# Kernel optimization log

Measured on AMD Instinct MI355X. Metric: run time of the kernel, lower is better.

## Reference

```python
import jax, jax.numpy as jnp
import numpy as np

D_MODEL = 128
N_HEADS = 8
RES_SCALE = 2.0 ** (-0.5)  # self_normalizing residual scale

OCC = np.array([65,66,67,68,69,70,71,72,73,74,75,76,77,81,82,83,84,88,89,90,94], dtype=np.int64)


def conv1d_same(x, w, groups=1):
    # x: [B, Cin, T], w: [Cout, Cin//groups, K] -> [B, Cout, T], 'same' padding, no bias
    return jax.lax.conv_general_dilated(
        x, w, window_strides=(1,), padding='SAME',
        dimension_numbers=('NCH', 'OIH', 'NCH'),
        feature_group_count=groups)


def setup_inputs() -> dict:
    key = jax.random.key(0)
    ks = jax.random.split(key, 7)
    B, C, T = 8, 128, 500
    L, D, O, K = 2, D_MODEL, 21, 9
    def lecun(k, shape, fan_in):
        return jax.random.normal(k, shape, dtype=jnp.float32) / jnp.sqrt(jnp.float32(fan_in))
    return {
        'x': jax.random.normal(ks[0], (B, C, T), dtype=jnp.float32),
        'occ_idx': jnp.asarray(OCC),
        'wq': lecun(ks[1], (L, D, O, K), O * K),
        'wk': lecun(ks[2], (L, C * D, 1, K), K),
        'wv': lecun(ks[3], (L, C * D, 1, K), K),
        'wproj': lecun(ks[4], (L, C, D), D),
        'w_head': lecun(ks[5], (40, C * T), C * T),
        'b_head': jnp.zeros((40,), dtype=jnp.float32),
    }


def reference(x, occ_idx, wq, wk, wv, wproj, w_head, b_head):
    B, C, T = x.shape
    L = wq.shape[0]
    H, D = N_HEADS, D_MODEL
    d = D // H  # head dim
    scale = d ** (-0.5)
    selu = jax.nn.selu
    for l in range(L):
        x_occ = x[:, occ_idx]                               # [B, O, T]
        Q = selu(conv1d_same(x_occ, wq[l]))                 # [B, D, T]
        K = selu(conv1d_same(x, wk[l], groups=C))           # [B, C*D, T]
        V = selu(conv1d_same(x, wv[l], groups=C))           # [B, C*D, T]
        Qh = Q.reshape(B, H, d, T)                          # b (h d) t -> b h d t
        Kh = K.reshape(B, C, H, d, T).transpose(0, 2, 1, 3, 4)  # b h c d t
        Vh = V.reshape(B, C, H, d, T).transpose(0, 2, 1, 3, 4)
        gates = selu(jnp.einsum('bhdt,bhcdt->bhct', Qh, Kh) * scale)
        out = jnp.einsum('bhct,bhcdt->bhcdt', gates, Vh)    # [B, H, C, d, T]
        out = out.transpose(0, 2, 1, 3, 4).reshape(B, C, D, T)  # b (c h d) t grouped by c
        # grouped 1x1 conv (groups=C): per-channel projection D -> 1
        out = selu(jnp.einsum('bcdt,cd->bct', out, wproj[l]))
        x = (x + out) * RES_SCALE
    logits = x.reshape(B, -1) @ w_head.T + b_head           # [B, n_classes]
    return logits
```

## Files before the change

kernel.cpp:

```cpp
#include <hip/hip_runtime.h>
#include <math.h>

#define T_LEN   500
#define C_CH    128
#define DM      128
#define N_OCC   21
#define KSZ     9
#define N_OUT   40
#define LOG2E   1.44269504088896340736f

typedef _Float16 f16x8 __attribute__((ext_vector_type(8)));
typedef _Float16 f16x2 __attribute__((ext_vector_type(2)));
typedef float    f32x16 __attribute__((ext_vector_type(16)));

union pair_u { unsigned int u; f16x2 h; };

__device__ __forceinline__ float exp2_fast(float y) {
#if __has_builtin(__builtin_amdgcn_exp2f)
    return __builtin_amdgcn_exp2f(y);
#else
    return exp2f(y);
#endif
}

__device__ __forceinline__ float selu2(float y) {
    const float c1 = 0.7282904300f;
    const float la = 1.7580993408473766f;
    float e = exp2_fast(y);
    return y > 0.f ? c1 * y : fmaf(la, e, -la);
}

__device__ __forceinline__ f32x16 zero16() {
    f32x16 z;
#pragma unroll
    for (int j = 0; j < 16; ++j) z[j] = 0.f;
    return z;
}

__global__ void prep_kernel(const float* __restrict__ wq,
                            const float* __restrict__ wk, const float* __restrict__ wv,
                            float* __restrict__ wqT,
                            _Float16* __restrict__ wkh, _Float16* __restrict__ wvh)
{
    int idx = blockIdx.x * 256 + threadIdx.x;
    if (idx < 2 * N_OCC * KSZ * DM) {
        int D  = idx & 127;
        int r  = idx >> 7;
        int k  = r % KSZ;
        int r2 = r / KSZ;
        int o  = r2 % N_OCC;
        int l  = r2 / N_OCC;
        wqT[idx] = wq[(((size_t)l * DM + D) * N_OCC + o) * KSZ + k] * LOG2E;
    }
    if (idx < 2 * C_CH * 4 * 64) {
        int lane = idx & 63;
        int ch   = (idx >> 6) & 3;
        int c    = (idx >> 8) & 127;
        int l    = idx >> 15;
        int tcol = lane & 31, hi = lane >> 5;
        int D    = ch * 32 + tcol;
        const float* wkp = wk + ((size_t)l * C_CH * DM + (size_t)c * DM + D) * KSZ;
        const float* wvp = wv + ((size_t)l * C_CH * DM + (size_t)c * DM + D) * KSZ;
#pragma unroll
        for (int j = 0; j < 8; ++j) {
            int k = 8 * hi + j;
            wkh[(size_t)idx * 8 + j] = (k < KSZ) ? (_Float16)(wkp[k] * LOG2E) : (_Float16)0.f;
            wvh[(size_t)idx * 8 + j] = (k < KSZ) ? (_Float16)(wvp[k] * LOG2E) : (_Float16)0.f;
        }
    }
}

#define ATCH 8
__global__ __launch_bounds__(128) void qconv_kernel(
    const float* __restrict__ xin, const int* __restrict__ occ,
    const float* __restrict__ wqT, float* __restrict__ qtP, int l)
{
    const int b  = blockIdx.y;
    const int t0 = blockIdx.x * ATCH;
    const int D  = threadIdx.x;
    __shared__ float xo[N_OCC][ATCH + 8];
    for (int i = threadIdx.x; i < N_OCC * (ATCH + 8); i += 128) {
        int o = i / (ATCH + 8), j = i % (ATCH + 8);
        int tg = t0 + j - 4;
        xo[o][j] = (tg >= 0 && tg < T_LEN)
                     ? xin[((size_t)b * C_CH + occ[o]) * T_LEN + tg] : 0.f;
    }
    __syncthreads();

    float acc[ATCH];
#pragma unroll
    for (int tt = 0; tt < ATCH; ++tt) acc[tt] = 0.f;

    for (int o = 0; o < N_OCC; ++o) {
        float xr[ATCH + 8];
#pragma unroll
        for (int j = 0; j < ATCH + 8; ++j) xr[j] = xo[o][j];
#pragma unroll
        for (int k = 0; k < KSZ; ++k) {
            float w = wqT[(((size_t)l * N_OCC + o) * KSZ + k) * DM + D];
#pragma unroll
            for (int tt = 0; tt < ATCH; ++tt)
                acc[tt] = fmaf(xr[tt + k], w, acc[tt]);
        }
    }
    const int tile = t0 >> 5, tl = t0 & 31;
    const int ch = D >> 5, w = D & 31;
    const int g  = 2 * (w >> 3) + ((w >> 2) & 1);
    const int i2 = w & 3;
    float* qb = qtP + ((((size_t)(b * 16 + tile) * 4 + ch) * 8 + g) * 32 + tl) * 4 + i2;
#pragma unroll
    for (int tt = 0; tt < ATCH; ++tt)
        if (t0 + tt < T_LEN) qb[tt * 4] = selu2(acc[tt]);
}

__global__ __launch_bounds__(256) void fused_layer(
    const float* __restrict__ xin, const float* __restrict__ qtP,
    const f16x8* __restrict__ wkh, const f16x8* __restrict__ wvh,
    const float* __restrict__ wproj, float* __restrict__ xout, int l)
{
    const int c = blockIdx.x, b = blockIdx.y;
    const int tid  = threadIdx.x;
    const int wave = tid >> 6;
    const int lane = tid & 63;
    const int tcol = lane & 31;
    const int hi   = lane >> 5;

    const f16x8* wkf = wkh + ((size_t)(l * C_CH + c) * 4) * 64 + lane;
    const f16x8* wvf = wvh + ((size_t)(l * C_CH + c) * 4) * 64 + lane;
    f16x8 ak[4], av[4];
#pragma unroll
    for (int ch = 0; ch < 4; ++ch) {
        ak[ch] = wkf[ch * 64];
        av[ch] = wvf[ch * 64];
    }

    __shared__ float xs[528];
    __shared__ unsigned int xs2[527];
    __shared__ float wpj[DM];
    const float* xp = xin + ((size_t)(b * C_CH + c)) * T_LEN;
    for (int i = tid; i < 528; i += 256) {
        int tg = i - 4;
        float a0 = (tg >= 0 && tg < T_LEN) ? xp[tg] : 0.f;
        float a1 = (tg + 1 >= 0 && tg + 1 < T_LEN) ? xp[tg + 1] : 0.f;
        xs[i] = a0;
        if (i < 527) {
            pair_u p;
            p.h[0] = (_Float16)a0;
            p.h[1] = (_Float16)a1;
            xs2[i] = p.u;
        }
    }
    if (tid < DM) wpj[tid] = wproj[((size_t)l * C_CH + c) * DM + tid];
    __syncthreads();

#define LOADQ(p0, p1, p2, p3, chv, tilev) do {                                \
    const float4* qp_ = reinterpret_cast<const float4*>(qtP)                  \
        + (((size_t)(b * 16 + (tilev)) * 4 + (chv)) * 8) * 32 + tcol;         \
    p0 = qp_[(0 + hi) * 32];                                                  \
    p1 = qp_[(2 + hi) * 32];                                                  \
    p2 = qp_[(4 + hi) * 32];                                                  \
    p3 = qp_[(6 + hi) * 32];                                                  \
} while (0)

#define KPROC(chv, p0, p1, p2, p3) do {                                       \
    f32x16 acc_ = zero16();                                                   \
    acc_ = __builtin_amdgcn_mfma_f32_32x32x16_f16(ak[chv], bfr, acc_, 0, 0, 0);\
    float pA = 0.f, pB = 0.f;                                                 \
    pA = fmaf(p0.x, selu2(acc_[0]),  pA);                                     \
    pA = fmaf(p0.y, selu2(acc_[1]),  pA);                                     \
    pA = fmaf(p0.z, selu2(acc_[2]),  pA);                                     \
    pA = fmaf(p0.w, selu2(acc_[3]),  pA);                                     \
    pA = fmaf(p1.x, selu2(acc_[4]),  pA);                                     \
    pA = fmaf(p1.y, selu2(acc_[5]),  pA);                                     \
    pA = fmaf(p1.z, selu2(acc_[6]),  pA);                                     \
    pA = fmaf(p1.w, selu2(acc_[7]),  pA);                                     \
    pB = fmaf(p2.x, selu2(acc_[8]),  pB);                                     \
    pB = fmaf(p2.y, selu2(acc_[9]),  pB);                                     \
    pB = fmaf(p2.z, selu2(acc_[10]), pB);                                     \
    pB = fmaf(p2.w, selu2(acc_[11]), pB);                                     \
    pB = fmaf(p3.x, selu2(acc_[12]), pB);                                     \
    pB = fmaf(p3.y, selu2(acc_[13]), pB);                                     \
    pB = fmaf(p3.z, selu2(acc_[14]), pB);                                     \
    pB = fmaf(p3.w, selu2(acc_[15]), pB);                                     \
    qk[(chv) * 2 + 0] += pA;                                                  \
    qk[(chv) * 2 + 1] += pB;                                                  \
} while (0)

    float4 qa0, qa1, qa2, qa3, qb0, qb1, qb2, qb3;
    LOADQ(qa0, qa1, qa2, qa3, 0, wave * 4);
    LOADQ(qb0, qb1, qb2, qb3, 1, wave * 4);

#pragma unroll 1
    for (int ti = 0; ti < 4; ++ti) {
        const int tile = wave * 4 + ti;
        const int loc0 = tile * 32;
        const int t    = loc0 + tcol;

        f16x8 bfr;
        {
            const int base = loc0 + tcol + 8 * hi;
#pragma unroll
            for (int j = 0; j < 4; ++j) {
                pair_u p; p.u = xs2[base + 2 * j];
                bfr[2 * j]     = p.h[0];
                bfr[2 * j + 1] = p.h[1];
            }
        }

        float qk[8];
#pragma unroll
        for (int h = 0; h < 8; ++h) qk[h] = 0.f;

        KPROC(0, qa0, qa1, qa2, qa3);
        LOADQ(qa0, qa1, qa2, qa3, 2, tile);
        KPROC(1, qb0, qb1, qb2, qb3);
        LOADQ(qb0, qb1, qb2, qb3, 3, tile);
        KPROC(2, qa0, qa1, qa2, qa3);
        KPROC(3, qb0, qb1, qb2, qb3);

        float g[8];
#pragma unroll
        for (int h = 0; h < 8; ++h) {
            float full = qk[h] + __shfl_xor(qk[h], 32);
            g[h] = selu2(full * (0.25f * LOG2E));
        }

        const int ntile = (ti < 3) ? tile + 1 : tile;
        LOADQ(qa0, qa1, qa2, qa3, 0, ntile);
        LOADQ(qb0, qb1, qb2, qb3, 1, ntile);

        float outp = 0.f;
#pragma unroll
        for (int ch = 0; ch < 4; ++ch) {
            f32x16 acc = zero16();
            acc = __builtin_amdgcn_mfma_f32_32x32x16_f16(av[ch], bfr, acc, 0, 0, 0);
            float sA = 0.f, sB = 0.f;
#pragma unroll
            for (int I = 0; I < 4; ++I) {
                float4 wq4 = *reinterpret_cast<const float4*>(
                    &wpj[(ch * 8 + 2 * I + hi) * 4]);
#pragma unroll
                for (int i2 = 0; i2 < 4; ++i2) {
                    float vv = selu2(acc[4 * I + i2]);
                    if (I < 2) sA = fmaf((&wq4.x)[i2], vv, sA);
                    else       sB = fmaf((&wq4.x)[i2], vv, sB);
                }
            }
            outp = fmaf(g[ch * 2 + 0], sA, outp);
            outp = fmaf(g[ch * 2 + 1], sB, outp);
        }
        float outf = outp + __shfl_xor(outp, 32);

        if (hi == 0 && t < T_LEN) {
            const float rs = 0.70710678118654752f;
            xout[((size_t)(b * C_CH + c)) * T_LEN + t]
                = (xs[loc0 + tcol + 4] + selu2(outf * LOG2E)) * rs;
        }
    }
#undef LOADQ
#undef KPROC
}

#define NCHUNK 16
#define CHUNK  (C_CH * T_LEN / NCHUNK)
__global__ __launch_bounds__(256) void head_partial(
    const float* __restrict__ x, const float* __restrict__ wh,
    float* __restrict__ part)
{
    const int o  = blockIdx.x;
    const int ch = blockIdx.y;
    const int base = ch * CHUNK;
    const float4* wp = reinterpret_cast<const float4*>(wh + (size_t)o * (C_CH * T_LEN) + base);

    float acc[8];
#pragma unroll
    for (int b = 0; b < 8; ++b) acc[b] = 0.f;

    for (int i = threadIdx.x; i < CHUNK / 4; i += 256) {
        float4 w4 = wp[i];
#pragma unroll
        for (int b = 0; b < 8; ++b) {
            float4 x4 = reinterpret_cast<const float4*>(
                x + (size_t)b * (C_CH * T_LEN) + base)[i];
            acc[b] = fmaf(x4.x, w4.x, acc[b]);
            acc[b] = fmaf(x4.y, w4.y, acc[b]);
            acc[b] = fmaf(x4.z, w4.z, acc[b]);
            acc[b] = fmaf(x4.w, w4.w, acc[b]);
        }
    }

#pragma unroll
    for (int b = 0; b < 8; ++b)
#pragma unroll
        for (int off = 32; off > 0; off >>= 1)
            acc[b] += __shfl_down(acc[b], off);

    __shared__ float red[4][8];
    const int lane = threadIdx.x & 63, wid = threadIdx.x >> 6;
    if (lane == 0)
#pragma unroll
        for (int b = 0; b < 8; ++b) red[wid][b] = acc[b];
    __syncthreads();
    if (threadIdx.x < 8) {
        int b = threadIdx.x;
        part[((size_t)o * NCHUNK + ch) * 8 + b]
            = red[0][b] + red[1][b] + red[2][b] + red[3][b];
    }
}

__global__ __launch_bounds__(320) void head_final(
    const float* __restrict__ part, const float* __restrict__ bh,
    float* __restrict__ out)
{
    int i = threadIdx.x;
    if (i >= N_OUT * 8) return;
    int o = i >> 3, b = i & 7;
    float s = bh[o];
#pragma unroll
    for (int ch = 0; ch < NCHUNK; ++ch)
        s += part[((size_t)o * NCHUNK + ch) * 8 + b];
    out[b * N_OUT + o] = s;
}

extern "C" void kernel_launch(void* const* d_in, const int* in_sizes, int n_in,
                              void* d_out, int out_size, void* d_ws, size_t ws_size,
                              hipStream_t stream) {
    const float* x     = (const float*)d_in[0];
    const int*   occ   = (const int*)  d_in[1];
    const float* wq    = (const float*)d_in[2];
    const float* wk    = (const float*)d_in[3];
    const float* wv    = (const float*)d_in[4];
    const float* wproj = (const float*)d_in[5];
    const float* wh    = (const float*)d_in[6];
    const float* bh    = (const float*)d_in[7];
    float* out = (float*)d_out;

    float* ws  = (float*)d_ws;
    float* wqT = ws;
    float* qtb = wqT + 2 * N_OCC * KSZ * DM;
    float* xb0 = qtb + (size_t)8 * 16 * DM * 32;
    float* xb1 = xb0 + (size_t)8 * C_CH * T_LEN;
    float* hp  = xb1 + (size_t)8 * C_CH * T_LEN;
    _Float16* wkh = (_Float16*)(hp + N_OUT * NCHUNK * 8);
    _Float16* wvh = wkh + (size_t)2 * C_CH * 4 * 64 * 8;

    prep_kernel<<<dim3(256), 256, 0, stream>>>(wq, wk, wv, wqT, wkh, wvh);

    qconv_kernel<<<dim3(63, 8), 128, 0, stream>>>(x, occ, wqT, qtb, 0);
    fused_layer <<<dim3(128, 8), 256, 0, stream>>>(
        x, qtb, (const f16x8*)wkh, (const f16x8*)wvh, wproj, xb0, 0);

    qconv_kernel<<<dim3(63, 8), 128, 0, stream>>>(xb0, occ, wqT, qtb, 1);
    fused_layer <<<dim3(128, 8), 256, 0, stream>>>(
        xb0, qtb, (const f16x8*)wkh, (const f16x8*)wvh, wproj, xb1, 1);

    head_partial<<<dim3(N_OUT, NCHUNK), 256, 0, stream>>>(xb1, wh, hp);
    head_final  <<<dim3(1), 320, 0, stream>>>(hp, bh, out);
}
```

Measured before the change: 112.5 us.

## Split fused layer over time halves and fold head reduction into atomics

The fused attention layer now launches twice as many blocks, each handling half of the time axis with two tiles per wave instead of four. This is meant to raise occupancy across the GPU's compute units, at the cost of duplicating the per-block weight register loads and halo staging. The Q prefetch schedule is reordered to suit the shorter loop. The two-kernel head is also replaced by a memset plus one kernel that accumulates partials with atomicAdd, which removes a launch but makes the float summation order nondeterministic.

```diff
diff --git a/kernel.cpp b/kernel.cpp
--- a/kernel.cpp
+++ b/kernel.cpp
@@ -118,7 +118,7 @@
     const f16x8* __restrict__ wkh, const f16x8* __restrict__ wvh,
     const float* __restrict__ wproj, float* __restrict__ xout, int l)
 {
-    const int c = blockIdx.x, b = blockIdx.y;
+    const int c = blockIdx.x, b = blockIdx.y, zi = blockIdx.z;
     const int tid  = threadIdx.x;
     const int wave = tid >> 6;
     const int lane = tid & 63;
@@ -134,16 +134,16 @@
         av[ch] = wvf[ch * 64];
     }
 
-    __shared__ float xs[528];
-    __shared__ unsigned int xs2[527];
+    __shared__ float xs[272];
+    __shared__ unsigned int xs2[271];
     __shared__ float wpj[DM];
     const float* xp = xin + ((size_t)(b * C_CH + c)) * T_LEN;
-    for (int i = tid; i < 528; i += 256) {
-        int tg = i - 4;
+    for (int i = tid; i < 272; i += 256) {
+        int tg = zi * 256 + i - 4;
         float a0 = (tg >= 0 && tg < T_LEN) ? xp[tg] : 0.f;
         float a1 = (tg + 1 >= 0 && tg + 1 < T_LEN) ? xp[tg + 1] : 0.f;
         xs[i] = a0;
-        if (i < 527) {
+        if (i < 271) {
             pair_u p;
             p.h[0] = (_Float16)a0;
             p.h[1] = (_Float16)a1;
@@ -187,14 +187,15 @@
 } while (0)
 
     float4 qa0, qa1, qa2, qa3, qb0, qb1, qb2, qb3;
-    LOADQ(qa0, qa1, qa2, qa3, 0, wave * 4);
-    LOADQ(qb0, qb1, qb2, qb3, 1, wave * 4);
+    LOADQ(qa0, qa1, qa2, qa3, 0, zi * 8 + wave * 2);
 
 #pragma unroll 1
-    for (int ti = 0; ti < 4; ++ti) {
-        const int tile = wave * 4 + ti;
-        const int loc0 = tile * 32;
-        const int t    = loc0 + tcol;
+    for (int ti = 0; ti < 2; ++ti) {
+        const int tile = zi * 8 + wave * 2 + ti;
+        const int loc0 = wave * 64 + ti * 32;
+        const int t    = zi * 256 + loc0 + tcol;
+
+        LOADQ(qb0, qb1, qb2, qb3, 1, tile);
 
         f16x8 bfr;
         {
@@ -216,6 +217,8 @@
         KPROC(1, qb0, qb1, qb2, qb3);
         LOADQ(qb0, qb1, qb2, qb3, 3, tile);
         KPROC(2, qa0, qa1, qa2, qa3);
+        const int ntile = (ti < 1) ? tile + 1 : tile;
+        LOADQ(qa0, qa1, qa2, qa3, 0, ntile);
         KPROC(3, qb0, qb1, qb2, qb3);
 
         float g[8];
@@ -224,10 +227,6 @@
             float full = qk[h] + __shfl_xor(qk[h], 32);
             g[h] = selu2(full * (0.25f * LOG2E));
         }
-
-        const int ntile = (ti < 3) ? tile + 1 : tile;
-        LOADQ(qa0, qa1, qa2, qa3, 0, ntile);
-        LOADQ(qb0, qb1, qb2, qb3, 1, ntile);
 
         float outp = 0.f;
 #pragma unroll
@@ -263,9 +262,9 @@
 
 #define NCHUNK 16
 #define CHUNK  (C_CH * T_LEN / NCHUNK)
-__global__ __launch_bounds__(256) void head_partial(
+__global__ __launch_bounds__(256) void head_kernel(
     const float* __restrict__ x, const float* __restrict__ wh,
-    float* __restrict__ part)
+    const float* __restrict__ bh, float* __restrict__ out)
 {
     const int o  = blockIdx.x;
     const int ch = blockIdx.y;
@@ -303,23 +302,10 @@
     __syncthreads();
     if (threadIdx.x < 8) {
         int b = threadIdx.x;
-        part[((size_t)o * NCHUNK + ch) * 8 + b]
-            = red[0][b] + red[1][b] + red[2][b] + red[3][b];
-    }
-}
-
-__global__ __launch_bounds__(320) void head_final(
-    const float* __restrict__ part, const float* __restrict__ bh,
-    float* __restrict__ out)
-{
-    int i = threadIdx.x;
-    if (i >= N_OUT * 8) return;
-    int o = i >> 3, b = i & 7;
-    float s = bh[o];
-#pragma unroll
-    for (int ch = 0; ch < NCHUNK; ++ch)
-        s += part[((size_t)o * NCHUNK + ch) * 8 + b];
-    out[b * N_OUT + o] = s;
+        float v = red[0][b] + red[1][b] + red[2][b] + red[3][b];
+        if (ch == 0) v += bh[o];
+        atomicAdd(&out[b * N_OUT + o], v);
+    }
 }
 
 extern "C" void kernel_launch(void* const* d_in, const int* in_sizes, int n_in,
@@ -340,20 +326,19 @@
     float* qtb = wqT + 2 * N_OCC * KSZ * DM;
     float* xb0 = qtb + (size_t)8 * 16 * DM * 32;
     float* xb1 = xb0 + (size_t)8 * C_CH * T_LEN;
-    float* hp  = xb1 + (size_t)8 * C_CH * T_LEN;
-    _Float16* wkh = (_Float16*)(hp + N_OUT * NCHUNK * 8);
+    _Float16* wkh = (_Float16*)(xb1 + (size_t)8 * C_CH * T_LEN);
     _Float16* wvh = wkh + (size_t)2 * C_CH * 4 * 64 * 8;
 
     prep_kernel<<<dim3(256), 256, 0, stream>>>(wq, wk, wv, wqT, wkh, wvh);
 
     qconv_kernel<<<dim3(63, 8), 128, 0, stream>>>(x, occ, wqT, qtb, 0);
-    fused_layer <<<dim3(128, 8), 256, 0, stream>>>(
+    fused_layer <<<dim3(128, 8, 2), 256, 0, stream>>>(
         x, qtb, (const f16x8*)wkh, (const f16x8*)wvh, wproj, xb0, 0);
 
     qconv_kernel<<<dim3(63, 8), 128, 0, stream>>>(xb0, occ, wqT, qtb, 1);
-    fused_layer <<<dim3(128, 8), 256, 0, stream>>>(
+    fused_layer <<<dim3(128, 8, 2), 256, 0, stream>>>(
         xb0, qtb, (const f16x8*)wkh, (const f16x8*)wvh, wproj, xb1, 1);
 
-    head_partial<<<dim3(N_OUT, NCHUNK), 256, 0, stream>>>(xb1, wh, hp);
-    head_final  <<<dim3(1), 320, 0, stream>>>(hp, bh, out);
-}
+    hipMemsetAsync(out, 0, (size_t)out_size * sizeof(float), stream);
+    head_kernel<<<dim3(N_OUT, NCHUNK), 256, 0, stream>>>(xb1, wh, bh, out);
+}
```

New measurement: 120.9 us. +7.5%, slower.
